# Kernel tuning notes

Measured on AMD Instinct MI355X. Metric: run time of the kernel, lower is better.

Reference implementation:

```python
import jax, jax.numpy as jnp
import numpy as np

N_BOND = 100000      # number of 'bond' nodes in the batched graph
IN_DIM = 32
SPACE_NUM = 6
D = SPACE_NUM * IN_DIM  # 192; bo_merge='cat' keeps h at space_num*in_dim
N_ETYPES = 36        # len(prot_atom_ids) * len(drug_atom_ids) = 4 * 9
E_PER_TYPE = 30000   # edges per edge type
B = 256              # batch_size (number of graphs)


def setup_inputs() -> dict:
    key = jax.random.key(0)
    k1, k2, k3, k4, k5 = jax.random.split(key, 5)
    h = jax.random.normal(k1, (N_BOND, D), dtype=jnp.float32)
    # output_layer: nn.Linear(D, 1, bias=False)
    W_out = jax.random.normal(k2, (D, 1), dtype=jnp.float32) / np.sqrt(D)
    # per-edge-type source node ids (DGL copy_u gather indices)
    edge_src = jax.random.randint(k3, (N_ETYPES, E_PER_TYPE), 0, N_BOND, dtype=jnp.int32)
    # per-edge graph id; sorted within each type (mimics arange(B).repeat(batch_num_edges))
    edge_seg = jnp.sort(jax.random.randint(k4, (N_ETYPES, E_PER_TYPE), 0, B, dtype=jnp.int32), axis=1)
    mask_mat = jax.random.randint(k5, (B, N_ETYPES), 0, 2).astype(bool)
    return {"h": h, "W_out": W_out, "edge_src": edge_src,
            "edge_seg": edge_seg, "mask_mat": mask_mat}


def reference(h, W_out, edge_src, edge_seg, mask_mat):
    # Fused over all 36 edge types: global segment id = type * B + graph_id
    type_idx = jnp.arange(N_ETYPES, dtype=edge_seg.dtype)[:, None]        # [T,1]
    seg_global = (type_idx * B + edge_seg).reshape(-1)                    # [T*E]
    eh = h[edge_src.reshape(-1)]                                          # gather: [T*E, D]
    sums = jax.ops.segment_sum(eh, seg_global, num_segments=N_ETYPES * B)  # [T*B, D]
    graph_feat = sums.reshape(N_ETYPES, B, D).transpose(1, 0, 2)          # [B, T, D]
    graph_v = jnp.einsum('btd,do->bt', graph_feat, W_out)                 # [B, T]
    graph_v = jnp.where(mask_mat, jnp.float32(-1e9), graph_v)
    return jax.nn.softmax(graph_v, axis=1)
```

## Files before the change

kernel.cpp:

```cpp
#include <hip/hip_runtime.h>

#define N_BOND   100000
#define D_DIM    192
#define N_ETYPES 36
#define E_PER_TYPE 30000
#define BATCH    256
#define TOTAL_E  (N_ETYPES * E_PER_TYPE)

__global__ void hv_kernel(const float* __restrict__ h, const float* __restrict__ W,
                          float* __restrict__ hv) {
    int gwave = (blockIdx.x * blockDim.x + threadIdx.x) >> 6;
    int lane  = threadIdx.x & 63;
    if (gwave >= N_BOND) return;
    float v = 0.f;
    if (lane < 48) {
        const float4 a = ((const float4*)(h + (size_t)gwave * D_DIM))[lane];
        const float4 w = ((const float4*)W)[lane];
        v = a.x * w.x + a.y * w.y + a.z * w.z + a.w * w.w;
    }
#pragma unroll
    for (int d = 32; d > 0; d >>= 1) v += __shfl_down(v, d, 64);
    if (lane == 0) hv[gwave] = v;
}

__global__ void edge_kernel(const int* __restrict__ edge_src,
                            const int* __restrict__ edge_seg,
                            const float* __restrict__ hv,
                            float* __restrict__ acc) {
    int e    = blockIdx.x * blockDim.x + threadIdx.x;
    int lane = threadIdx.x & 63;
    bool valid = (e < TOTAL_E);
    int ec  = valid ? e : (TOTAL_E - 1);
    int t   = ec / E_PER_TYPE;
    int seg = edge_seg[ec];
    int src = edge_src[ec];
    float val = valid ? hv[src] : 0.0f;
    int key = t * BATCH + seg;

#pragma unroll
    for (int d = 1; d < 64; d <<= 1) {
        float uv = __shfl_up(val, d, 64);
        int   uk = __shfl_up(key, d, 64);
        if (lane >= d && uk == key) val += uv;
    }
    int nk = __shfl_down(key, 1, 64);
    if (lane == 63 || nk != key) atomicAdd(&acc[key], val);
}

__global__ void softmax_kernel(const float* __restrict__ acc,
                               const void* __restrict__ mask,
                               float* __restrict__ out) {
    int b = threadIdx.x;

    const unsigned int* mi = (const unsigned int*)mask;
    bool is_u8 = false;
#pragma unroll
    for (int i = 0; i < 16; ++i) is_u8 |= (mi[i] > 1u);
    const unsigned char* m8  = (const unsigned char*)mask;
    const int*           m32 = (const int*)mask;

    float v[N_ETYPES];
    float mx = -1e30f;
#pragma unroll
    for (int t = 0; t < N_ETYPES; ++t) {
        float x = acc[t * BATCH + b];
        bool masked = is_u8 ? (m8[b * N_ETYPES + t] != 0)
                            : (m32[b * N_ETYPES + t] != 0);
        x = masked ? -1e9f : x;
        v[t] = x;
        mx = fmaxf(mx, x);
    }
    float s = 0.f;
#pragma unroll
    for (int t = 0; t < N_ETYPES; ++t) { v[t] = expf(v[t] - mx); s += v[t]; }
    float inv = 1.f / s;
#pragma unroll
    for (int t = 0; t < N_ETYPES; ++t) out[b * N_ETYPES + t] = v[t] * inv;
}

extern "C" void kernel_launch(void* const* d_in, const int* in_sizes, int n_in,
                              void* d_out, int out_size, void* d_ws, size_t ws_size,
                              hipStream_t stream) {
    const float* h        = (const float*)d_in[0];
    const float* W        = (const float*)d_in[1];
    const int*   edge_src = (const int*)d_in[2];
    const int*   edge_seg = (const int*)d_in[3];
    const void*  mask     = d_in[4];
    float*       out      = (float*)d_out;

    float* hv  = (float*)d_ws;
    float* acc = (float*)((char*)d_ws + 400128);

    hipMemsetAsync(acc, 0, N_ETYPES * BATCH * sizeof(float), stream);

    hipLaunchKernelGGL(hv_kernel, dim3((N_BOND + 3) / 4), dim3(256), 0, stream, h, W, hv);

    int eb = (TOTAL_E + 255) / 256;
    hipLaunchKernelGGL(edge_kernel, dim3(eb), dim3(256), 0, stream, edge_src, edge_seg, hv, acc);

    hipLaunchKernelGGL(softmax_kernel, dim3(1), dim3(256), 0, stream, acc, mask, out);
}
```

Measured before the change: 140.0 us.

## Fold acc zeroing into hv kernel, pack 4 rows per wave, vectorize edge loads

Drops the separate memset by having the hv kernel zero the accumulator. The hv kernel now gives each row a quarter-wave (16 lanes × 3 float4) instead of a full wave with idle lanes. The edge kernel handles 4 edges per thread with int4 loads and merges runs locally before the wave segmented scan, which cuts the thread count and the number of atomics. The per-thread local merge can issue extra atomics at segment boundaries. Correctness relies on each 4-edge group staying within one edge type, which holds because 30000 is divisible by 4.

```diff
diff --git a/kernel.cpp b/kernel.cpp
--- a/kernel.cpp
+++ b/kernel.cpp
@@ -6,45 +6,68 @@
 #define E_PER_TYPE 30000
 #define BATCH    256
 #define TOTAL_E  (N_ETYPES * E_PER_TYPE)
+#define ACC_N    (N_ETYPES * BATCH)
 
 __global__ void hv_kernel(const float* __restrict__ h, const float* __restrict__ W,
-                          float* __restrict__ hv) {
-    int gwave = (blockIdx.x * blockDim.x + threadIdx.x) >> 6;
-    int lane  = threadIdx.x & 63;
-    if (gwave >= N_BOND) return;
+                          float* __restrict__ hv, float* __restrict__ acc) {
+    int gid = blockIdx.x * blockDim.x + threadIdx.x;
+    if (gid < ACC_N) acc[gid] = 0.f;
+
+    int wave = gid >> 6;
+    int lane = threadIdx.x & 63;
+    int row  = wave * 4 + (lane >> 4);
+    int ql   = lane & 15;
+    if (row >= N_BOND) return;
+
+    const float4* hp = (const float4*)(h + (size_t)row * D_DIM);
+    const float4* wp = (const float4*)W;
     float v = 0.f;
-    if (lane < 48) {
-        const float4 a = ((const float4*)(h + (size_t)gwave * D_DIM))[lane];
-        const float4 w = ((const float4*)W)[lane];
-        v = a.x * w.x + a.y * w.y + a.z * w.z + a.w * w.w;
+#pragma unroll
+    for (int k = 0; k < 3; ++k) {
+        float4 a = hp[ql + 16 * k];
+        float4 w = wp[ql + 16 * k];
+        v += a.x * w.x + a.y * w.y + a.z * w.z + a.w * w.w;
     }
 #pragma unroll
-    for (int d = 32; d > 0; d >>= 1) v += __shfl_down(v, d, 64);
-    if (lane == 0) hv[gwave] = v;
+    for (int d = 8; d > 0; d >>= 1) v += __shfl_down(v, d, 64);
+    if (ql == 0) hv[row] = v;
 }
 
 __global__ void edge_kernel(const int* __restrict__ edge_src,
                             const int* __restrict__ edge_seg,
                             const float* __restrict__ hv,
                             float* __restrict__ acc) {
-    int e    = blockIdx.x * blockDim.x + threadIdx.x;
+    int tid  = blockIdx.x * blockDim.x + threadIdx.x;
     int lane = threadIdx.x & 63;
-    bool valid = (e < TOTAL_E);
-    int ec  = valid ? e : (TOTAL_E - 1);
-    int t   = ec / E_PER_TYPE;
-    int seg = edge_seg[ec];
-    int src = edge_src[ec];
-    float val = valid ? hv[src] : 0.0f;
-    int key = t * BATCH + seg;
+    int e0   = tid * 4;
+    bool valid = (e0 < TOTAL_E);
+    int ec = valid ? e0 : (TOTAL_E - 4);
+    int t  = ec / E_PER_TYPE;
+
+    int4 s4 = ((const int4*)edge_seg)[ec >> 2];
+    int4 r4 = ((const int4*)edge_src)[ec >> 2];
+    float v0 = valid ? hv[r4.x] : 0.f;
+    float v1 = valid ? hv[r4.y] : 0.f;
+    float v2 = valid ? hv[r4.z] : 0.f;
+    float v3 = valid ? hv[r4.w] : 0.f;
+
+    int base = t * BATCH;
+    int k0 = base + s4.x, k1 = base + s4.y, k2 = base + s4.z, k3 = base + s4.w;
+
+    int   ck = k0;
+    float cv = v0;
+    if (k1 == ck) cv += v1; else { atomicAdd(&acc[ck], cv); ck = k1; cv = v1; }
+    if (k2 == ck) cv += v2; else { atomicAdd(&acc[ck], cv); ck = k2; cv = v2; }
+    if (k3 == ck) cv += v3; else { atomicAdd(&acc[ck], cv); ck = k3; cv = v3; }
 
 #pragma unroll
     for (int d = 1; d < 64; d <<= 1) {
-        float uv = __shfl_up(val, d, 64);
-        int   uk = __shfl_up(key, d, 64);
-        if (lane >= d && uk == key) val += uv;
+        float uv = __shfl_up(cv, d, 64);
+        int   uk = __shfl_up(ck, d, 64);
+        if (lane >= d && uk == ck) cv += uv;
     }
-    int nk = __shfl_down(key, 1, 64);
-    if (lane == 63 || nk != key) atomicAdd(&acc[key], val);
+    int nk = __shfl_down(ck, 1, 64);
+    if (lane == 63 || nk != ck) atomicAdd(&acc[ck], cv);
 }
 
 __global__ void softmax_kernel(const float* __restrict__ acc,
@@ -91,11 +114,9 @@
     float* hv  = (float*)d_ws;
     float* acc = (float*)((char*)d_ws + 400128);
 
-    hipMemsetAsync(acc, 0, N_ETYPES * BATCH * sizeof(float), stream);
+    hipLaunchKernelGGL(hv_kernel, dim3(N_BOND / 16), dim3(256), 0, stream, h, W, hv, acc);
 
-    hipLaunchKernelGGL(hv_kernel, dim3((N_BOND + 3) / 4), dim3(256), 0, stream, h, W, hv);
-
-    int eb = (TOTAL_E + 255) / 256;
+    int eb = (TOTAL_E / 4 + 255) / 256;
     hipLaunchKernelGGL(edge_kernel, dim3(eb), dim3(256), 0, stream, edge_src, edge_seg, hv, acc);
 
     hipLaunchKernelGGL(softmax_kernel, dim3(1), dim3(256), 0, stream, acc, mask, out);
```

After: 130.9 us. -6.6%, faster.
